# Kernel optimization log

Measured on AMD Instinct MI355X. Metric: run time of the kernel, lower is better.

Reference implementation:

```python
import jax, jax.numpy as jnp
import numpy as np

H = 256          # lstm_size
VOCAB = 6        # num_branches + 1
NBR = 5          # num_branches
TEMP = 5.0
OP_TANH = 1.1 / 2.5
BLOCKS, SEQ = 16, 2048


def setup_inputs() -> dict:
    key = jax.random.key(0)
    ks = jax.random.split(key, 12)
    def gw(k, shape, scale=0.05):
        return jax.random.normal(k, shape, dtype=jnp.float32) * scale
    return {
        "arc": jax.random.randint(ks[0], (BLOCKS, SEQ), 0, VOCAB, dtype=jnp.int32),
        "h0": gw(ks[1], (2, 1, H), 0.01),
        "c0": gw(ks[2], (2, 1, H), 0.01),
        "emb": gw(ks[3], (VOCAB, H)),
        "Wih_f": gw(ks[4], (4 * H, H)), "Whh_f": gw(ks[5], (4 * H, H)),
        "bih_f": jnp.zeros(4 * H, jnp.float32), "bhh_f": jnp.zeros(4 * H, jnp.float32),
        "Wih_b": gw(ks[6], (4 * H, H)), "Whh_b": gw(ks[7], (4 * H, H)),
        "bih_b": jnp.zeros(4 * H, jnp.float32), "bhh_b": jnp.zeros(4 * H, jnp.float32),
        "fcW": gw(ks[8], (NBR, 2 * H)), "fcb": jnp.zeros(NBR, jnp.float32),
    }


def _lstm_dir(x, h0, c0, Wih, Whh, bih, bhh):
    # x: [T,H]; one direction of a 1-layer LSTM, PyTorch gate order (i,f,g,o)
    def step(carry, xt):
        h, c = carry
        g = xt @ Wih.T + h @ Whh.T + bih + bhh          # [4H]
        i, f, gg, o = jnp.split(g, 4)
        i, f, o = jax.nn.sigmoid(i), jax.nn.sigmoid(f), jax.nn.sigmoid(o)
        c = f * c + i * jnp.tanh(gg)
        h = o * jnp.tanh(c)
        return (h, c), h
    (hT, cT), hs = jax.lax.scan(step, (h0, c0), x)
    return hs, hT, cT


def reference(arc, h0, c0, emb, Wih_f, Whh_f, bih_f, bhh_f,
              Wih_b, Whh_b, bih_b, bhh_b, fcW, fcb):
    key0 = jax.random.key(42)

    def block(carry, arc_i):
        hf, cf, hb, cb, key = carry
        key, sub = jax.random.split(key)
        x = emb[arc_i]                                   # [T,H]
        hs_f, hfT, cfT = _lstm_dir(x, hf, cf, Wih_f, Whh_f, bih_f, bhh_f)
        hs_b, hbT, cbT = _lstm_dir(x[::-1], hb, cb, Wih_b, Whh_b, bih_b, bhh_b)
        out = jnp.concatenate([hs_f, hs_b[::-1]], axis=-1)   # [T,2H]
        logits = (out @ fcW.T + fcb) / TEMP
        logits = OP_TANH * jnp.tanh(logits)              # [T,5]
        logp = jax.nn.log_softmax(logits, axis=-1)
        prob = jnp.exp(logp)
        idx = jax.random.categorical(sub, logits, axis=-1)   # multinomial(softmax(logits))
        # F.cross_entropy(logits, idx) == mean NLL of sampled indices
        ce = -jnp.mean(jnp.take_along_axis(logp, idx[:, None], axis=-1))
        # original: -mean(sum(logp*prob over size-1 dim)) == -mean over [T,5]
        ent = jax.lax.stop_gradient(-jnp.mean(logp * prob))
        return (hfT, cfT, hbT, cbT, key), (idx, ce, ent)

    init = (h0[0, 0], c0[0, 0], h0[1, 0], c0[1, 0], key0)
    (hfT, cfT, hbT, cbT, _), (all_arc, ces, ents) = jax.lax.scan(block, init, arc)
    h = jnp.stack([hfT, hbT])[:, None, :]                # [2,1,H]
    c = jnp.stack([cfT, cbT])[:, None, :]
    return all_arc, jnp.sum(ces), jnp.sum(ents), h, c
```

## Files before the change

kernel.cpp:

```cpp
#include <hip/hip_runtime.h>
#include <math.h>
#include <stdint.h>

static constexpr int XG_OFF   = 0;
static constexpr int MB_OFF   = 12288;
static constexpr int SH_OFF   = 20480;
static constexpr int SC_OFF   = 20992;
static constexpr int HIST_OFF = 21504;
static constexpr int HIST_D   = 524288;
static constexpr int CEP_OFF  = 1070080;
static constexpr int ENTP_OFF = 1070144;

static constexpr int OUT_CE = 32768;
static constexpr int OUT_H  = 32770;
static constexpr int OUT_C  = 33282;

__device__ __forceinline__ uint32_t rotl32(uint32_t v, int n) {
  return (v << n) | (v >> (32 - n));
}
__device__ __forceinline__ void tf2x32(uint32_t k0, uint32_t k1,
                                       uint32_t x0, uint32_t x1,
                                       uint32_t& y0, uint32_t& y1) {
  const uint32_t k2 = k0 ^ k1 ^ 0x1BD11BDAu;
  x0 += k0; x1 += k1;
  x0 += x1; x1 = rotl32(x1, 13); x1 ^= x0;
  x0 += x1; x1 = rotl32(x1, 15); x1 ^= x0;
  x0 += x1; x1 = rotl32(x1, 26); x1 ^= x0;
  x0 += x1; x1 = rotl32(x1, 6);  x1 ^= x0;
  x0 += k1; x1 += k2 + 1u;
  x0 += x1; x1 = rotl32(x1, 17); x1 ^= x0;
  x0 += x1; x1 = rotl32(x1, 29); x1 ^= x0;
  x0 += x1; x1 = rotl32(x1, 16); x1 ^= x0;
  x0 += x1; x1 = rotl32(x1, 24); x1 ^= x0;
  x0 += k2; x1 += k0 + 2u;
  x0 += x1; x1 = rotl32(x1, 13); x1 ^= x0;
  x0 += x1; x1 = rotl32(x1, 15); x1 ^= x0;
  x0 += x1; x1 = rotl32(x1, 26); x1 ^= x0;
  x0 += x1; x1 = rotl32(x1, 6);  x1 ^= x0;
  x0 += k0; x1 += k1 + 3u;
  x0 += x1; x1 = rotl32(x1, 17); x1 ^= x0;
  x0 += x1; x1 = rotl32(x1, 29); x1 ^= x0;
  x0 += x1; x1 = rotl32(x1, 16); x1 ^= x0;
  x0 += x1; x1 = rotl32(x1, 24); x1 ^= x0;
  x0 += k1; x1 += k2 + 4u;
  x0 += x1; x1 = rotl32(x1, 13); x1 ^= x0;
  x0 += x1; x1 = rotl32(x1, 15); x1 ^= x0;
  x0 += x1; x1 = rotl32(x1, 26); x1 ^= x0;
  x0 += x1; x1 = rotl32(x1, 6);  x1 ^= x0;
  x0 += k2; x1 += k0 + 5u;
  y0 = x0; y1 = x1;
}

__device__ __forceinline__ float gumbel_from_bits(uint32_t bits) {
  float f = __uint_as_float(0x3f800000u | (bits >> 9)) - 1.0f;
  const float tiny = __uint_as_float(0x00800000u);
  float u = fmaxf(tiny, f + tiny);
  float l1 = (float)log((double)u);
  return -(float)log(-(double)l1);
}

__global__ void k_xg(const float* __restrict__ emb,
                     const float* __restrict__ WihF, const float* __restrict__ bihF,
                     const float* __restrict__ bhhF,
                     const float* __restrict__ WihB, const float* __restrict__ bihB,
                     const float* __restrict__ bhhB,
                     float* __restrict__ ws) {
  __shared__ float se[1536];
  const int tid = threadIdx.x;
  for (int i = tid; i < 1536; i += 256) se[i] = emb[i];
  __syncthreads();
  const int gid = blockIdx.x * 256 + tid;
  const int d = gid >> 10, r = gid & 1023;
  const float* Wih = d ? WihB : WihF;
  const float* bih = d ? bihB : bihF;
  const float* bhh = d ? bhhB : bhhF;
  float acc[6] = {0.f, 0.f, 0.f, 0.f, 0.f, 0.f};
  const float4* wr = (const float4*)(Wih + r * 256);
  for (int c = 0; c < 64; c++) {
    float4 wv = wr[c];
#pragma unroll
    for (int v = 0; v < 6; v++) {
      const float* ev = &se[v * 256 + 4 * c];
      acc[v] += wv.x * ev[0] + wv.y * ev[1] + wv.z * ev[2] + wv.w * ev[3];
    }
  }
  const float bsum = bih[r] + bhh[r];
#pragma unroll
  for (int v = 0; v < 6; v++) ws[XG_OFF + d * 6144 + v * 1024 + r] = acc[v] + bsum;
}

__global__ __launch_bounds__(256, 1)
void k_chain(const int* __restrict__ arc, const float* __restrict__ h0,
             const float* __restrict__ c0, const float* __restrict__ WhhF,
             const float* __restrict__ WhhB, float* __restrict__ ws,
             float* __restrict__ out, int b) {
  const int tid = threadIdx.x;
  const int d = blockIdx.x >> 3;
  const int k = blockIdx.x & 7;
  const int w = tid >> 6;
  const int lane = tid & 63;
  const int q = lane >> 4, p = lane & 15;

  __shared__ float xg_l[768];
  __shared__ int arc_s[2048];
  __shared__ float h_s[16 * 20];
  __shared__ float gate_l[128];

  const float* Whh = d ? WhhB : WhhF;
  for (int i = tid; i < 768; i += 256) {
    const int sym = i >> 7, r = i & 127, gw = r >> 5, e = r & 31;
    xg_l[i] = ws[XG_OFF + d * 6144 + sym * 1024 + gw * 256 + 32 * k + e];
  }
  {
    const int* ab = arc + b * 2048;
    for (int i = tid; i < 2048; i += 256) arc_s[i] = ab[i];
  }
  float4 W[8][4];
  const int e0 = 32 * k + 8 * q;
#pragma unroll
  for (int i = 0; i < 8; i++) {
    const float* rp = Whh + (256 * w + e0 + i) * 256 + 16 * p;
#pragma unroll
    for (int j = 0; j < 4; j++) W[i][j] = ((const float4*)rp)[j];
  }
  h_s[(tid >> 4) * 20 + (tid & 15)] =
      (b == 0) ? h0[d * 256 + tid] : ws[SH_OFF + d * 256 + tid];
  float cval = 0.f, hval = 0.f;
  if (tid < 32)
    cval = (b == 0) ? c0[d * 256 + 32 * k + tid] : ws[SC_OFF + d * 256 + 32 * k + tid];
  __syncthreads();
  float4 hw[4];
  {
    const float4* hp = (const float4*)&h_s[p * 20];
#pragma unroll
    for (int j = 0; j < 4; j++) hw[j] = hp[j];
  }
  unsigned long long* mb = (unsigned long long*)(ws + MB_OFF);
  const unsigned stampBase = (unsigned)b * 2048u;
  const bool writer = (p < 8);
  float* histD = ws + HIST_OFF + d * HIST_D;
  const bool selfPoll = ((tid >> 5) == k);

  for (int t = 0; t < 2048; t++) {
    float acc[8];
#pragma unroll
    for (int i = 0; i < 8; i++) {
      float a;
      a  = W[i][0].x * hw[0].x;
      a += W[i][0].y * hw[0].y;
      a += W[i][0].z * hw[0].z;
      a += W[i][0].w * hw[0].w;
      a += W[i][1].x * hw[1].x;
      a += W[i][1].y * hw[1].y;
      a += W[i][1].z * hw[1].z;
      a += W[i][1].w * hw[1].w;
      a += W[i][2].x * hw[2].x;
      a += W[i][2].y * hw[2].y;
      a += W[i][2].z * hw[2].z;
      a += W[i][2].w * hw[2].w;
      a += W[i][3].x * hw[3].x;
      a += W[i][3].y * hw[3].y;
      a += W[i][3].z * hw[3].z;
      a += W[i][3].w * hw[3].w;
      acc[i] = a;
    }
#pragma unroll
    for (int i = 0; i < 8; i++) {
      float v = acc[i];
      v += __shfl_xor(v, 1, 16);
      v += __shfl_xor(v, 2, 16);
      v += __shfl_xor(v, 4, 16);
      v += __shfl_xor(v, 8, 16);
      acc[i] = v;
    }
    if (writer) {
      float g = acc[0];
      g = (p == 1) ? acc[1] : g;
      g = (p == 2) ? acc[2] : g;
      g = (p == 3) ? acc[3] : g;
      g = (p == 4) ? acc[4] : g;
      g = (p == 5) ? acc[5] : g;
      g = (p == 6) ? acc[6] : g;
      g = (p == 7) ? acc[7] : g;
      gate_l[w * 32 + 8 * q + p] = g;
    }
    __syncthreads();

    const unsigned stamp = stampBase + (unsigned)t + 1u;
    unsigned long long* mbp = mb + (d * 2 + (t & 1)) * 256;
    if (tid < 32) {
      const int sym = arc_s[d ? (2047 - t) : t];
      const float* xgs = &xg_l[sym * 128];
      const float gi = gate_l[tid]      + xgs[tid];
      const float gf = gate_l[32 + tid] + xgs[32 + tid];
      const float gg = gate_l[64 + tid] + xgs[64 + tid];
      const float go = gate_l[96 + tid] + xgs[96 + tid];
      const float I = 1.0f / (1.0f + expf(-gi));
      const float F = 1.0f / (1.0f + expf(-gf));
      const float G = tanhf(gg);
      const float O = 1.0f / (1.0f + expf(-go));
      cval = F * cval + I * G;
      hval = O * tanhf(cval);
      const int e = 32 * k + tid;
      h_s[(e >> 4) * 20 + (e & 15)] = hval;
      histD[t * 256 + e] = hval;
      const unsigned long long pk = (unsigned long long)__float_as_uint(hval) |
                                    ((unsigned long long)stamp << 32);
      __hip_atomic_store(&mbp[e], pk, __ATOMIC_RELAXED, __HIP_MEMORY_SCOPE_AGENT);
    }
    {
      unsigned long long v;
      for (;;) {
        v = __hip_atomic_load(&mbp[tid], __ATOMIC_RELAXED, __HIP_MEMORY_SCOPE_AGENT);
        bool ok = selfPoll | ((unsigned)(v >> 32) == stamp);
        if (__all(ok)) break;
      }
      if (!selfPoll) h_s[(tid >> 4) * 20 + (tid & 15)] = __uint_as_float((unsigned)v);
    }
    __syncthreads();
    {
      const float4* hp = (const float4*)&h_s[p * 20];
#pragma unroll
      for (int j = 0; j < 4; j++) hw[j] = hp[j];
    }
  }

  if (tid < 32) {
    const int e = 32 * k + tid;
    ws[SH_OFF + d * 256 + e] = hval;
    ws[SC_OFF + d * 256 + e] = cval;
    if (b == 15) {
      out[OUT_H + d * 256 + e] = hval;
      out[OUT_C + d * 256 + e] = cval;
    }
  }
}

__global__ void k_sampler(const float* __restrict__ fcW, const float* __restrict__ fcb,
                          float* __restrict__ ws, float* __restrict__ out, int b) {
  const int tid = threadIdx.x;
  __shared__ float sW[5 * 512];
  __shared__ float sb[5];
  __shared__ float red[256];
  for (int i = tid; i < 2560; i += 256) sW[i] = fcW[i];
  if (tid < 5) sb[tid] = fcb[tid];
  __syncthreads();
  uint32_t s0 = 0u, s1 = 0u;
  {
    uint32_t k0 = 0u, k1 = 42u;
    for (int i = 0; i <= b; i++) {
      uint32_t n0, n1, t0, t1;
      tf2x32(k0, k1, 0u, 0u, n0, n1);
      tf2x32(k0, k1, 0u, 1u, t0, t1);
      s0 = t0; s1 = t1;
      k0 = n0; k1 = n1;
    }
  }
  const int pp = blockIdx.x * 256 + tid;
  const float* histF = ws + HIST_OFF;
  const float* histB = ws + HIST_OFF + HIST_D;
  float dotL[5] = {0.f, 0.f, 0.f, 0.f, 0.f};
  float dotH[5] = {0.f, 0.f, 0.f, 0.f, 0.f};
  const float4* hfL = (const float4*)(histF + pp * 256);
  const float4* hbL = (const float4*)(histB + (2047 - pp) * 256);
  const float4* hfH = (const float4*)(histF + (pp + 1024) * 256);
  const float4* hbH = (const float4*)(histB + (1023 - pp) * 256);
  for (int c = 0; c < 64; c++) {
    float4 a = hfL[c], bb = hbL[c], e = hfH[c], f = hbH[c];
#pragma unroll
    for (int j = 0; j < 5; j++) {
      const float* wr = &sW[j * 512 + 4 * c];
      dotL[j] += a.x * wr[0] + a.y * wr[1] + a.z * wr[2] + a.w * wr[3];
      dotL[j] += bb.x * wr[256] + bb.y * wr[257] + bb.z * wr[258] + bb.w * wr[259];
      dotH[j] += e.x * wr[0] + e.y * wr[1] + e.z * wr[2] + e.w * wr[3];
      dotH[j] += f.x * wr[256] + f.y * wr[257] + f.z * wr[258] + f.w * wr[259];
    }
  }
  uint32_t bl[5], bh[5];
#pragma unroll
  for (int j = 0; j < 5; j++) {
    uint32_t y0, y1;
    tf2x32(s0, s1, 0u, (uint32_t)(5 * pp + j), y0, y1);
    bl[j] = y0 ^ y1;
    tf2x32(s0, s1, 0u, (uint32_t)(5 * (pp + 1024) + j), y0, y1);
    bh[j] = y0 ^ y1;
  }
  const float OPT = (float)(1.1 / 2.5);
  float ce_acc = 0.f, ent_acc = 0.f;
#pragma unroll
  for (int half = 0; half < 2; half++) {
    const int t = half ? (pp + 1024) : pp;
    float l[5];
#pragma unroll
    for (int j = 0; j < 5; j++) {
      float dv = half ? dotH[j] : dotL[j];
      l[j] = OPT * tanhf((dv + sb[j]) / 5.0f);
    }
    int idx = 0;
    float best;
    {
      uint32_t b0 = half ? bh[0] : bl[0];
      best = gumbel_from_bits(b0) + l[0];
    }
#pragma unroll
    for (int j = 1; j < 5; j++) {
      uint32_t bj = half ? bh[j] : bl[j];
      float v = gumbel_from_bits(bj) + l[j];
      if (v > best) { best = v; idx = j; }
    }
    out[b * 2048 + t] = (float)idx;
    float m = l[0];
#pragma unroll
    for (int j = 1; j < 5; j++) m = fmaxf(m, l[j]);
    float ssum = 0.f;
#pragma unroll
    for (int j = 0; j < 5; j++) ssum += expf(l[j] - m);
    float lse = logf(ssum);
    float lpidx = 0.f;
#pragma unroll
    for (int j = 0; j < 5; j++) {
      float lp = (l[j] - m) - lse;
      ent_acc -= lp * expf(lp);
      lpidx = (j == idx) ? lp : lpidx;
    }
    ce_acc -= lpidx;
  }
  red[tid] = ce_acc; __syncthreads();
  for (int s = 128; s > 0; s >>= 1) {
    if (tid < s) red[tid] += red[tid + s];
    __syncthreads();
  }
  if (tid == 0) ws[CEP_OFF + b * 4 + blockIdx.x] = red[0];
  __syncthreads();
  red[tid] = ent_acc; __syncthreads();
  for (int s = 128; s > 0; s >>= 1) {
    if (tid < s) red[tid] += red[tid + s];
    __syncthreads();
  }
  if (tid == 0) ws[ENTP_OFF + b * 4 + blockIdx.x] = red[0];
}

__global__ void k_final(const float* __restrict__ ws, float* __restrict__ out) {
  if (threadIdx.x == 0 && blockIdx.x == 0) {
    float ce = 0.f, ent = 0.f;
    for (int b = 0; b < 16; b++) {
      float cb = 0.f, eb = 0.f;
      for (int j = 0; j < 4; j++) {
        cb += ws[CEP_OFF + b * 4 + j];
        eb += ws[ENTP_OFF + b * 4 + j];
      }
      ce += cb / 2048.0f;
      ent += eb / 10240.0f;
    }
    out[OUT_CE] = ce;
    out[OUT_CE + 1] = ent;
  }
}

extern "C" void kernel_launch(void* const* d_in, const int* in_sizes, int n_in,
                              void* d_out, int out_size, void* d_ws, size_t ws_size,
                              hipStream_t stream) {
  (void)in_sizes; (void)n_in; (void)out_size; (void)ws_size;
  const int* arc = (const int*)d_in[0];
  const float* h0 = (const float*)d_in[1];
  const float* c0 = (const float*)d_in[2];
  const float* emb = (const float*)d_in[3];
  const float* WihF = (const float*)d_in[4];
  const float* WhhF = (const float*)d_in[5];
  const float* bihF = (const float*)d_in[6];
  const float* bhhF = (const float*)d_in[7];
  const float* WihB = (const float*)d_in[8];
  const float* WhhB = (const float*)d_in[9];
  const float* bihB = (const float*)d_in[10];
  const float* bhhB = (const float*)d_in[11];
  const float* fcW = (const float*)d_in[12];
  const float* fcb = (const float*)d_in[13];
  float* out = (float*)d_out;
  float* ws = (float*)d_ws;

  hipLaunchKernelGGL(k_xg, dim3(8), dim3(256), 0, stream,
                     emb, WihF, bihF, bhhF, WihB, bihB, bhhB, ws);
  for (int b = 0; b < 16; b++) {
    hipLaunchKernelGGL(k_chain, dim3(16), dim3(256), 0, stream,
                       arc, h0, c0, WhhF, WhhB, ws, out, b);
    hipLaunchKernelGGL(k_sampler, dim3(4), dim3(256), 0, stream,
                       fcW, fcb, ws, out, b);
  }
  hipLaunchKernelGGL(k_final, dim3(1), dim3(64), 0, stream, ws, out);
}
```

Before: 67.57 ms.

## Remap gate rows so each quad owns full cell, drop mid-step barrier

Reassigns the recurrent weight rows so each 16-lane group computes all four gates (i,f,g,o) for two hidden elements. The cell update then happens redundantly in registers instead of through a shared gate buffer, which removes one __syncthreads per timestep. The xg table is relaid out so a thread can fetch its gate biases with float4 loads. h_s becomes double-buffered, and the mailbox poll is now per-thread (skipping self-polling warps) with two loads per iteration instead of a wave-wide __all. This trims the latency of the serial chain at the cost of redundant transcendental math across lanes.

Measured after the change: 69.58 ms. 3.0% more time.

```diff
diff --git a/kernel.cpp b/kernel.cpp
--- a/kernel.cpp
+++ b/kernel.cpp
@@ -103,41 +103,40 @@
 
   __shared__ float xg_l[768];
   __shared__ int arc_s[2048];
-  __shared__ float h_s[16 * 20];
-  __shared__ float gate_l[128];
+  __shared__ float h_s[2][256];
 
   const float* Whh = d ? WhhB : WhhF;
   for (int i = tid; i < 768; i += 256) {
-    const int sym = i >> 7, r = i & 127, gw = r >> 5, e = r & 31;
-    xg_l[i] = ws[XG_OFF + d * 6144 + sym * 1024 + gw * 256 + 32 * k + e];
+    const int sym = i >> 7, r = i & 127, el = r >> 2, g = r & 3;
+    xg_l[i] = ws[XG_OFF + d * 6144 + sym * 1024 + g * 256 + 32 * k + el];
   }
   {
     const int* ab = arc + b * 2048;
     for (int i = tid; i < 2048; i += 256) arc_s[i] = ab[i];
   }
+  const int eA = 32 * k + 8 * w + 2 * q;
+  const int elA = 8 * w + 2 * q;
   float4 W[8][4];
-  const int e0 = 32 * k + 8 * q;
 #pragma unroll
   for (int i = 0; i < 8; i++) {
-    const float* rp = Whh + (256 * w + e0 + i) * 256 + 16 * p;
+    const int R = 256 * (i >> 1) + eA + (i & 1);
+    const float* rp = Whh + R * 256 + 16 * p;
 #pragma unroll
     for (int j = 0; j < 4; j++) W[i][j] = ((const float4*)rp)[j];
   }
-  h_s[(tid >> 4) * 20 + (tid & 15)] =
-      (b == 0) ? h0[d * 256 + tid] : ws[SH_OFF + d * 256 + tid];
-  float cval = 0.f, hval = 0.f;
-  if (tid < 32)
-    cval = (b == 0) ? c0[d * 256 + 32 * k + tid] : ws[SC_OFF + d * 256 + 32 * k + tid];
+  h_s[0][tid] = (b == 0) ? h0[d * 256 + tid] : ws[SH_OFF + d * 256 + tid];
+  float cA = (b == 0) ? c0[d * 256 + eA] : ws[SC_OFF + d * 256 + eA];
+  float cB = (b == 0) ? c0[d * 256 + eA + 1] : ws[SC_OFF + d * 256 + eA + 1];
+  float hA = 0.f, hB = 0.f;
   __syncthreads();
   float4 hw[4];
   {
-    const float4* hp = (const float4*)&h_s[p * 20];
+    const float4* hp = (const float4*)&h_s[0][16 * p];
 #pragma unroll
     for (int j = 0; j < 4; j++) hw[j] = hp[j];
   }
   unsigned long long* mb = (unsigned long long*)(ws + MB_OFF);
   const unsigned stampBase = (unsigned)b * 2048u;
-  const bool writer = (p < 8);
   float* histD = ws + HIST_OFF + d * HIST_D;
   const bool selfPoll = ((tid >> 5) == k);
 
@@ -173,65 +172,73 @@
       v += __shfl_xor(v, 8, 16);
       acc[i] = v;
     }
-    if (writer) {
-      float g = acc[0];
-      g = (p == 1) ? acc[1] : g;
-      g = (p == 2) ? acc[2] : g;
-      g = (p == 3) ? acc[3] : g;
-      g = (p == 4) ? acc[4] : g;
-      g = (p == 5) ? acc[5] : g;
-      g = (p == 6) ? acc[6] : g;
-      g = (p == 7) ? acc[7] : g;
-      gate_l[w * 32 + 8 * q + p] = g;
-    }
-    __syncthreads();
-
-    const unsigned stamp = stampBase + (unsigned)t + 1u;
-    unsigned long long* mbp = mb + (d * 2 + (t & 1)) * 256;
-    if (tid < 32) {
-      const int sym = arc_s[d ? (2047 - t) : t];
-      const float* xgs = &xg_l[sym * 128];
-      const float gi = gate_l[tid]      + xgs[tid];
-      const float gf = gate_l[32 + tid] + xgs[32 + tid];
-      const float gg = gate_l[64 + tid] + xgs[64 + tid];
-      const float go = gate_l[96 + tid] + xgs[96 + tid];
+    const int sym = arc_s[d ? (2047 - t) : t];
+    const float4 xgA = *(const float4*)&xg_l[sym * 128 + elA * 4];
+    const float4 xgB = *(const float4*)&xg_l[sym * 128 + elA * 4 + 4];
+    {
+      const float gi = acc[0] + xgA.x;
+      const float gf = acc[2] + xgA.y;
+      const float gg = acc[4] + xgA.z;
+      const float go = acc[6] + xgA.w;
       const float I = 1.0f / (1.0f + expf(-gi));
       const float F = 1.0f / (1.0f + expf(-gf));
       const float G = tanhf(gg);
       const float O = 1.0f / (1.0f + expf(-go));
-      cval = F * cval + I * G;
-      hval = O * tanhf(cval);
-      const int e = 32 * k + tid;
-      h_s[(e >> 4) * 20 + (e & 15)] = hval;
-      histD[t * 256 + e] = hval;
-      const unsigned long long pk = (unsigned long long)__float_as_uint(hval) |
+      cA = F * cA + I * G;
+      hA = O * tanhf(cA);
+    }
+    {
+      const float gi = acc[1] + xgB.x;
+      const float gf = acc[3] + xgB.y;
+      const float gg = acc[5] + xgB.z;
+      const float go = acc[7] + xgB.w;
+      const float I = 1.0f / (1.0f + expf(-gi));
+      const float F = 1.0f / (1.0f + expf(-gf));
+      const float G = tanhf(gg);
+      const float O = 1.0f / (1.0f + expf(-go));
+      cB = F * cB + I * G;
+      hB = O * tanhf(cB);
+    }
+    const unsigned stamp = stampBase + (unsigned)t + 1u;
+    unsigned long long* mbp = mb + (d * 2 + (t & 1)) * 256;
+    const int np = (t + 1) & 1;
+    if (p < 2) {
+      const int e = eA + p;
+      const float hv = p ? hB : hA;
+      const unsigned long long pk = (unsigned long long)__float_as_uint(hv) |
                                     ((unsigned long long)stamp << 32);
       __hip_atomic_store(&mbp[e], pk, __ATOMIC_RELAXED, __HIP_MEMORY_SCOPE_AGENT);
-    }
-    {
+      histD[t * 256 + e] = hv;
+      h_s[np][e] = hv;
+    }
+    asm volatile("s_waitcnt vmcnt(0)" ::: "memory");
+    if (!selfPoll) {
       unsigned long long v;
       for (;;) {
-        v = __hip_atomic_load(&mbp[tid], __ATOMIC_RELAXED, __HIP_MEMORY_SCOPE_AGENT);
-        bool ok = selfPoll | ((unsigned)(v >> 32) == stamp);
-        if (__all(ok)) break;
+        unsigned long long v0 = __hip_atomic_load(&mbp[tid], __ATOMIC_RELAXED,
+                                                  __HIP_MEMORY_SCOPE_AGENT);
+        unsigned long long v1 = __hip_atomic_load(&mbp[tid], __ATOMIC_RELAXED,
+                                                  __HIP_MEMORY_SCOPE_AGENT);
+        if ((unsigned)(v0 >> 32) == stamp) { v = v0; break; }
+        if ((unsigned)(v1 >> 32) == stamp) { v = v1; break; }
       }
-      if (!selfPoll) h_s[(tid >> 4) * 20 + (tid & 15)] = __uint_as_float((unsigned)v);
+      h_s[np][tid] = __uint_as_float((unsigned)v);
     }
     __syncthreads();
     {
-      const float4* hp = (const float4*)&h_s[p * 20];
+      const float4* hp = (const float4*)&h_s[np][16 * p];
 #pragma unroll
       for (int j = 0; j < 4; j++) hw[j] = hp[j];
     }
   }
 
-  if (tid < 32) {
-    const int e = 32 * k + tid;
-    ws[SH_OFF + d * 256 + e] = hval;
-    ws[SC_OFF + d * 256 + e] = cval;
+  if (p < 2) {
+    const int e = eA + p;
+    ws[SH_OFF + d * 256 + e] = p ? hB : hA;
+    ws[SC_OFF + d * 256 + e] = p ? cB : cA;
     if (b == 15) {
-      out[OUT_H + d * 256 + e] = hval;
-      out[OUT_C + d * 256 + e] = cval;
+      out[OUT_H + d * 256 + e] = p ? hB : hA;
+      out[OUT_C + d * 256 + e] = p ? cB : cA;
     }
   }
 }
```
